# Optimization experiments

Hardware: AMD Instinct MI355X
Metric: run time of the kernel (lower is better)

Reference implementation:

```python
import jax, jax.numpy as jnp
import numpy as np

N_NODES = 100000
N_EDGES = 1600000
IN_F = 128
OUT_F = 128
HID = 2 * OUT_F  # 256


def setup_inputs() -> dict:
    key = jax.random.key(0)
    k1, k2, k3, k4, k5 = jax.random.split(key, 5)
    x = jax.random.normal(k1, (N_NODES, IN_F), dtype=jnp.float32)
    src = jax.random.randint(k2, (N_EDGES,), 0, N_NODES, dtype=jnp.int64)
    dst = jax.random.randint(k3, (N_EDGES,), 0, N_NODES, dtype=jnp.int64)
    # GraphConv params: glorot-style init, zero bias (as in dgl defaults)
    W1 = jax.random.normal(k4, (IN_F, HID), dtype=jnp.float32) / np.sqrt(IN_F)
    b1 = jnp.zeros((HID,), dtype=jnp.float32)
    W2 = jax.random.normal(k5, (HID, OUT_F), dtype=jnp.float32) / np.sqrt(HID)
    b2 = jnp.zeros((OUT_F,), dtype=jnp.float32)
    return {"x": x, "W1": W1, "b1": b1, "W2": W2, "b2": b2, "src": src, "dst": dst}


def _degree_norms(src, dst):
    ones = jnp.ones(src.shape[0], dtype=jnp.float32)
    out_deg = jax.ops.segment_sum(ones, src, num_segments=N_NODES)
    in_deg = jax.ops.segment_sum(ones, dst, num_segments=N_NODES)
    # dgl norm='both': deg^{-1/2}, with 0-degree clamped to 1
    out_norm = jnp.where(out_deg > 0, out_deg, 1.0) ** -0.5
    in_norm = jnp.where(in_deg > 0, in_deg, 1.0) ** -0.5
    return out_norm, in_norm


def _graph_conv(x, W, b, src, dst, out_norm, in_norm):
    # dgl GraphConv, norm='both': apply weight first if in_feats > out_feats
    h = x * out_norm[:, None]
    if W.shape[0] > W.shape[1]:
        h = h @ W                       # [N, out] -- shrink before aggregation
        agg = jax.ops.segment_sum(h[src], dst, num_segments=N_NODES)
        return agg * in_norm[:, None] + b
    else:
        agg = jax.ops.segment_sum(h[src], dst, num_segments=N_NODES)
        return (agg * in_norm[:, None]) @ W + b


def reference(x, W1, b1, W2, b2, src, dst):
    out_norm, in_norm = _degree_norms(src, dst)
    h = jax.nn.relu(_graph_conv(x, W1, b1, src, dst, out_norm, in_norm))
    h = jax.nn.relu(_graph_conv(h, W2, b2, src, dst, out_norm, in_norm))
    return h
```

## Files before the change

kernel.cpp:

```cpp
#include <hip/hip_runtime.h>
#include <stdint.h>

#define NNODES 100000
#define NEDGES 1600000
#define NBIN 391
#define EPB 4096
#define NB 391

typedef unsigned short bf16_t;
typedef __attribute__((ext_vector_type(8))) short bf16x8;
typedef __attribute__((ext_vector_type(8))) unsigned short u16x8;
typedef __attribute__((ext_vector_type(4))) float f32x4;

__device__ __forceinline__ float bf2f(unsigned short u) {
  return __uint_as_float(((unsigned)u) << 16);
}
__device__ __forceinline__ unsigned short f2bf(float f) {
  unsigned u = __float_as_uint(f);
  return (unsigned short)((u + 0x7FFFu + ((u >> 16) & 1u)) >> 16);
}
__device__ __forceinline__ void gload_lds16(const void* g, void* lds) {
  __builtin_amdgcn_global_load_lds(
      (const __attribute__((address_space(1))) unsigned int*)g,
      (__attribute__((address_space(3))) unsigned int*)lds, 16, 0, 0);
}

__global__ __launch_bounds__(256) void hist2_kernel(
    const int* __restrict__ src, const int* __restrict__ dst,
    int* __restrict__ cntD, int* __restrict__ cntS) {
  __shared__ int hD[NBIN], hS[NBIN];
  int blk = blockIdx.x, t = threadIdx.x;
  for (int i = t; i < NBIN; i += 256) { hD[i] = 0; hS[i] = 0; }
  __syncthreads();
  int e0 = blk * EPB + t * 16;
  if (e0 + 15 < NEDGES) {
#pragma unroll
    for (int q = 0; q < 4; q++) {
      int4 s4 = *reinterpret_cast<const int4*>(src + e0 + q * 4);
      int4 d4 = *reinterpret_cast<const int4*>(dst + e0 + q * 4);
      atomicAdd(&hD[d4.x >> 8], 1); atomicAdd(&hS[s4.x >> 8], 1);
      atomicAdd(&hD[d4.y >> 8], 1); atomicAdd(&hS[s4.y >> 8], 1);
      atomicAdd(&hD[d4.z >> 8], 1); atomicAdd(&hS[s4.z >> 8], 1);
      atomicAdd(&hD[d4.w >> 8], 1); atomicAdd(&hS[s4.w >> 8], 1);
    }
  } else {
    for (int e = e0; e < NEDGES && e < e0 + 16; e++) {
      atomicAdd(&hD[dst[e] >> 8], 1);
      atomicAdd(&hS[src[e] >> 8], 1);
    }
  }
  __syncthreads();
  for (int i = t; i < NBIN; i += 256) {
    cntD[(size_t)blk * NBIN + i] = hD[i];
    cntS[(size_t)blk * NBIN + i] = hS[i];
  }
}

__global__ __launch_bounds__(512) void scan_bin_kernel(
    int* __restrict__ cntD, int* __restrict__ cntS, int* __restrict__ binTot) {
  __shared__ int lds[512];
  int g = blockIdx.x, t = threadIdx.x;
  int* cnt = (g < NBIN) ? cntD : cntS;
  int gg = (g < NBIN) ? g : g - NBIN;
  int v = (t < NB) ? cnt[(size_t)t * NBIN + gg] : 0;
  lds[t] = v;
  __syncthreads();
  for (int off = 1; off < 512; off <<= 1) {
    int a = (t >= off) ? lds[t - off] : 0;
    __syncthreads();
    lds[t] += a;
    __syncthreads();
  }
  if (t < NB) cnt[(size_t)t * NBIN + gg] = lds[t] - v;
  if (t == 0) binTot[g] = lds[511];
}

__global__ __launch_bounds__(512) void base_wcast_kernel(
    const int* __restrict__ binTot, int* __restrict__ binbaseD,
    int* __restrict__ binbaseS, int* __restrict__ row_ptr,
    const float* __restrict__ W1, const float* __restrict__ W2,
    bf16_t* __restrict__ W1t, bf16_t* __restrict__ W2t) {
  if (blockIdx.x == 0) {
    __shared__ int lds[512];
    int t = threadIdx.x;
    int v = (t < NBIN) ? binTot[t] : 0;
    lds[t] = v;
    __syncthreads();
    for (int off = 1; off < 512; off <<= 1) {
      int a = (t >= off) ? lds[t - off] : 0;
      __syncthreads();
      lds[t] += a;
      __syncthreads();
    }
    if (t < NBIN) binbaseD[t] = lds[t] - v;
    if (t == NBIN - 1) { binbaseD[NBIN] = lds[t]; row_ptr[NNODES] = lds[t]; }
    __syncthreads();
    int v2 = (t < NBIN) ? binTot[NBIN + t] : 0;
    lds[t] = v2;
    __syncthreads();
    for (int off = 1; off < 512; off <<= 1) {
      int a = (t >= off) ? lds[t - off] : 0;
      __syncthreads();
      lds[t] += a;
      __syncthreads();
    }
    if (t < NBIN) binbaseS[t] = lds[t] - v2;
    if (t == NBIN - 1) binbaseS[NBIN] = lds[t];
  } else {
    int i = (blockIdx.x - 1) * 512 + threadIdx.x;
    if (i < 32768) {
      int n = i / 128, k = i % 128;
      W1t[i] = f2bf(W1[(size_t)k * 256 + n]);
    } else if (i < 65536) {
      int j = i - 32768;
      int n = j / 256, k = j % 256;
      W2t[j] = f2bf(W2[(size_t)k * 128 + n]);
    }
  }
}

__global__ __launch_bounds__(256) void scatter_recs_kernel(
    const int* __restrict__ src, const int* __restrict__ dst,
    const int* __restrict__ cntD, const int* __restrict__ cntS,
    const int* __restrict__ binbaseD, const int* __restrict__ binbaseS,
    unsigned int* __restrict__ recD, unsigned char* __restrict__ recS) {
  __shared__ int cD[NBIN], cS[NBIN];
  int blk = blockIdx.x, t = threadIdx.x;
  for (int i = t; i < NBIN; i += 256) {
    cD[i] = binbaseD[i] + cntD[(size_t)blk * NBIN + i];
    cS[i] = binbaseS[i] + cntS[(size_t)blk * NBIN + i];
  }
  __syncthreads();
  int e0 = blk * EPB + t * 16;
  if (e0 + 15 < NEDGES) {
#pragma unroll
    for (int q = 0; q < 4; q++) {
      int4 s4 = *reinterpret_cast<const int4*>(src + e0 + q * 4);
      int4 d4 = *reinterpret_cast<const int4*>(dst + e0 + q * 4);
      int ss[4] = {s4.x, s4.y, s4.z, s4.w};
      int dd[4] = {d4.x, d4.y, d4.z, d4.w};
#pragma unroll
      for (int i = 0; i < 4; i++) {
        int s = ss[i], d = dd[i];
        int pos = atomicAdd(&cD[d >> 8], 1);
        recD[pos] = ((unsigned)s << 8) | (unsigned)(d & 255);
        int ps = atomicAdd(&cS[s >> 8], 1);
        recS[ps] = (unsigned char)(s & 255);
      }
    }
  } else {
    for (int e = e0; e < NEDGES && e < e0 + 16; e++) {
      int s = src[e], d = dst[e];
      int pos = atomicAdd(&cD[d >> 8], 1);
      recD[pos] = ((unsigned)s << 8) | (unsigned)(d & 255);
      int ps = atomicAdd(&cS[s >> 8], 1);
      recS[ps] = (unsigned char)(s & 255);
    }
  }
}

__global__ __launch_bounds__(512) void finish2_kernel(
    const unsigned int* __restrict__ recD, const int* __restrict__ binbaseD,
    const unsigned char* __restrict__ recS, const int* __restrict__ binbaseS,
    int* __restrict__ row_ptr, float* __restrict__ in_norm, int* __restrict__ csr,
    float* __restrict__ out_norm, const float* __restrict__ x, bf16_t* __restrict__ xb) {
  __shared__ int hist[4096];
  __shared__ int cur[4096];
  __shared__ int sc[512];
  __shared__ float onv[256];
  int t = threadIdx.x;
  if (blockIdx.x < NBIN) {
    int b = blockIdx.x;
    int base = binbaseD[b];
    int cnt = binbaseD[b + 1] - base;
    for (int i = t; i < 4096; i += 512) hist[i] = 0;
    __syncthreads();
    const unsigned int* rec = recD + base;
    for (int i = t; i < cnt; i += 512) {
      unsigned int r = rec[i];
      atomicAdd(&hist[((r & 255u) << 4) | (r >> 21)], 1);
    }
    __syncthreads();
    int loc[8];
    int lsum = 0;
#pragma unroll
    for (int i = 0; i < 8; i++) { loc[i] = lsum; lsum += hist[t * 8 + i]; }
    sc[t] = lsum;
    __syncthreads();
    for (int off = 1; off < 512; off <<= 1) {
      int a = (t >= off) ? sc[t - off] : 0;
      __syncthreads();
      sc[t] += a;
      __syncthreads();
    }
    int toff = sc[t] - lsum;
#pragma unroll
    for (int i = 0; i < 8; i++) cur[t * 8 + i] = base + toff + loc[i];
    __syncthreads();
    if (t < 256) {
      int n = (b << 8) + t;
      if (n < NNODES) {
        row_ptr[n] = cur[t * 16];
        int v = 0;
#pragma unroll
        for (int p = 0; p < 16; p++) v += hist[t * 16 + p];
        in_norm[n] = rsqrtf((float)(v > 0 ? v : 1));
      }
    }
    __syncthreads();
    for (int i = t; i < cnt; i += 512) {
      unsigned int r = rec[i];
      int key = ((r & 255u) << 4) | (r >> 21);
      int slot = atomicAdd(&cur[key], 1);
      csr[slot] = (int)(r >> 8);
    }
  } else {
    int b = blockIdx.x - NBIN;
    int base = binbaseS[b];
    int cnt = binbaseS[b + 1] - base;
    if (t < 256) hist[t] = 0;
    __syncthreads();
    const unsigned char* rec = recS + base;
    for (int i = t; i < cnt; i += 512) atomicAdd(&hist[rec[i]], 1);
    __syncthreads();
    int n0 = b << 8;
    if (t < 256) {
      int v = hist[t];
      float on = rsqrtf((float)(v > 0 ? v : 1));
      onv[t] = on;
      int n = n0 + t;
      if (n < NNODES) out_norm[n] = on;
    }
    __syncthreads();
    for (int idx = t; idx < 256 * 16; idx += 512) {
      int r16 = idx >> 4, chunk = idx & 15;
      int n = n0 + r16;
      if (n >= NNODES) break;
      float s = onv[r16];
      const float4* xp = reinterpret_cast<const float4*>(x + (size_t)n * 128 + chunk * 8);
      float4 v0 = xp[0], v1 = xp[1];
      u16x8 u;
      u[0] = f2bf(v0.x * s); u[1] = f2bf(v0.y * s); u[2] = f2bf(v0.z * s); u[3] = f2bf(v0.w * s);
      u[4] = f2bf(v1.x * s); u[5] = f2bf(v1.y * s); u[6] = f2bf(v1.z * s); u[7] = f2bf(v1.w * s);
      *reinterpret_cast<u16x8*>(xb + (size_t)n * 128 + chunk * 8) = u;
    }
  }
}

template <int FIN>
__global__ __launch_bounds__(256) void gather_kernel(
    const bf16_t* __restrict__ feat, const int* __restrict__ row_ptr,
    const int* __restrict__ csr, const float* __restrict__ rs,
    const float* __restrict__ bias, void* __restrict__ outp) {
  int node = blockIdx.x * 16 + (threadIdx.x >> 4);
  int lane = threadIdx.x & 15;
  int start = row_ptr[node];
  int end = row_ptr[node + 1];
  float a[8];
#pragma unroll
  for (int t = 0; t < 8; t++) a[t] = 0.f;
  int j = start;
  for (; j + 7 < end; j += 8) {
    int4 sa = *reinterpret_cast<const int4*>(csr + j);
    int4 sb = *reinterpret_cast<const int4*>(csr + j + 4);
    u16x8 u0 = *reinterpret_cast<const u16x8*>(feat + (size_t)sa.x * 128 + lane * 8);
    u16x8 u1 = *reinterpret_cast<const u16x8*>(feat + (size_t)sa.y * 128 + lane * 8);
    u16x8 u2 = *reinterpret_cast<const u16x8*>(feat + (size_t)sa.z * 128 + lane * 8);
    u16x8 u3 = *reinterpret_cast<const u16x8*>(feat + (size_t)sa.w * 128 + lane * 8);
    u16x8 u4 = *reinterpret_cast<const u16x8*>(feat + (size_t)sb.x * 128 + lane * 8);
    u16x8 u5 = *reinterpret_cast<const u16x8*>(feat + (size_t)sb.y * 128 + lane * 8);
    u16x8 u6 = *reinterpret_cast<const u16x8*>(feat + (size_t)sb.z * 128 + lane * 8);
    u16x8 u7 = *reinterpret_cast<const u16x8*>(feat + (size_t)sb.w * 128 + lane * 8);
#pragma unroll
    for (int t = 0; t < 8; t++)
      a[t] += ((bf2f((unsigned short)u0[t]) + bf2f((unsigned short)u1[t])) +
               (bf2f((unsigned short)u2[t]) + bf2f((unsigned short)u3[t]))) +
              ((bf2f((unsigned short)u4[t]) + bf2f((unsigned short)u5[t])) +
               (bf2f((unsigned short)u6[t]) + bf2f((unsigned short)u7[t])));
  }
  if (j + 3 < end) {
    int4 sa = *reinterpret_cast<const int4*>(csr + j);
    u16x8 u0 = *reinterpret_cast<const u16x8*>(feat + (size_t)sa.x * 128 + lane * 8);
    u16x8 u1 = *reinterpret_cast<const u16x8*>(feat + (size_t)sa.y * 128 + lane * 8);
    u16x8 u2 = *reinterpret_cast<const u16x8*>(feat + (size_t)sa.z * 128 + lane * 8);
    u16x8 u3 = *reinterpret_cast<const u16x8*>(feat + (size_t)sa.w * 128 + lane * 8);
#pragma unroll
    for (int t = 0; t < 8; t++)
      a[t] += (bf2f((unsigned short)u0[t]) + bf2f((unsigned short)u1[t])) +
              (bf2f((unsigned short)u2[t]) + bf2f((unsigned short)u3[t]));
    j += 4;
  }
  for (; j < end; j++) {
    int s0 = csr[j];
    u16x8 u0 = *reinterpret_cast<const u16x8*>(feat + (size_t)s0 * 128 + lane * 8);
#pragma unroll
    for (int t = 0; t < 8; t++) a[t] += bf2f((unsigned short)u0[t]);
  }
  if (FIN == 0) {
    u16x8 o;
#pragma unroll
    for (int t = 0; t < 8; t++) o[t] = f2bf(a[t]);
    *reinterpret_cast<u16x8*>((bf16_t*)outp + (size_t)node * 128 + lane * 8) = o;
  } else {
    float s = rs[node];
    const float* bp = bias + lane * 8;
    float4 o0, o1;
    o0.x = fmaxf(fmaf(a[0], s, bp[0]), 0.f);
    o0.y = fmaxf(fmaf(a[1], s, bp[1]), 0.f);
    o0.z = fmaxf(fmaf(a[2], s, bp[2]), 0.f);
    o0.w = fmaxf(fmaf(a[3], s, bp[3]), 0.f);
    o1.x = fmaxf(fmaf(a[4], s, bp[4]), 0.f);
    o1.y = fmaxf(fmaf(a[5], s, bp[5]), 0.f);
    o1.z = fmaxf(fmaf(a[6], s, bp[6]), 0.f);
    o1.w = fmaxf(fmaf(a[7], s, bp[7]), 0.f);
    float* op = (float*)outp + (size_t)node * 128 + lane * 8;
    *reinterpret_cast<float4*>(op) = o0;
    *reinterpret_cast<float4*>(op + 4) = o1;
  }
}

__global__ __launch_bounds__(256) void gemm12_kernel(
    const bf16_t* __restrict__ A,
    const bf16_t* __restrict__ W1t,
    const bf16_t* __restrict__ W2t,
    const float* __restrict__ b1,
    const float* __restrict__ in_norm,
    const float* __restrict__ out_norm,
    bf16_t* __restrict__ s2b) {
  __shared__ __align__(16) bf16_t As[64 * 128];
  __shared__ __align__(16) bf16_t Wb[128 * 128];
  __shared__ __align__(16) bf16_t H[64 * 256];

  const int tid = threadIdx.x;
  const int lane = tid & 63;
  const int w = tid >> 6;
  const int m0 = blockIdx.x * 64;
  const int l15 = lane & 15;
  const int S = lane >> 4;
  const int r = w * 16 + l15;
  const int lr0 = w * 16 + S * 4;

#pragma unroll
  for (int p = 0; p < 4; p++) {
    int pos = p * 256 + tid;
    int rr = pos >> 4, slot = pos & 15;
    int row = m0 + rr; if (row > NNODES - 1) row = NNODES - 1;
    int ko = (slot ^ (rr & 7)) << 3;
    gload_lds16(A + (size_t)row * 128 + ko, &As[(p * 256 + w * 64) * 8]);
  }
#pragma unroll
  for (int p = 0; p < 8; p++) {
    int pos = p * 256 + tid;
    int n = pos >> 4, slot = pos & 15;
    int ko = (slot ^ (n & 7)) << 3;
    gload_lds16(W1t + (size_t)n * 128 + ko, &Wb[(p * 256 + w * 64) * 8]);
  }
  __syncthreads();

  float inn[4];
#pragma unroll
  for (int reg = 0; reg < 4; reg++) {
    int grow = m0 + lr0 + reg;
    inn[reg] = (grow < NNODES) ? in_norm[grow] : 1.0f;
  }

#pragma unroll
  for (int h = 0; h < 2; h++) {
    if (h == 1) {
      __syncthreads();
#pragma unroll
      for (int p = 0; p < 8; p++) {
        int pos = p * 256 + tid;
        int n = pos >> 4, slot = pos & 15;
        int ko = (slot ^ (n & 7)) << 3;
        gload_lds16(W1t + (size_t)(128 + n) * 128 + ko, &Wb[(p * 256 + w * 64) * 8]);
      }
      __syncthreads();
    }
    f32x4 acc1[8];
#pragma unroll
    for (int fn = 0; fn < 8; fn++) acc1[fn] = (f32x4){0.f, 0.f, 0.f, 0.f};
#pragma unroll
    for (int kk8 = 0; kk8 < 16; kk8 += 4) {
      bf16x8 af = *reinterpret_cast<const bf16x8*>(&As[r * 128 + (((kk8 + S) ^ (r & 7)) << 3)]);
#pragma unroll
      for (int fn = 0; fn < 8; fn++) {
        int n = fn * 16 + l15;
        bf16x8 bf = *reinterpret_cast<const bf16x8*>(&Wb[n * 128 + (((kk8 + S) ^ (n & 7)) << 3)]);
        acc1[fn] = __builtin_amdgcn_mfma_f32_16x16x32_bf16(af, bf, acc1[fn], 0, 0, 0);
      }
    }
#pragma unroll
    for (int fn = 0; fn < 8; fn++) {
      int col = h * 128 + fn * 16 + l15;
      float bb = b1[col];
#pragma unroll
      for (int reg = 0; reg < 4; reg++) {
        int lr = lr0 + reg;
        float v = fmaxf(fmaf(acc1[fn][reg], inn[reg], bb), 0.f);
        int slot = (col >> 3) ^ (lr & 7);
        H[lr * 256 + slot * 8 + (col & 7)] = f2bf(v);
      }
    }
  }
  __syncthreads();

  f32x4 acc2[8];
#pragma unroll
  for (int fn = 0; fn < 8; fn++) acc2[fn] = (f32x4){0.f, 0.f, 0.f, 0.f};
#pragma unroll
  for (int kh = 0; kh < 2; kh++) {
#pragma unroll
    for (int p = 0; p < 8; p++) {
      int pos = p * 256 + tid;
      int n = pos >> 4, slot = pos & 15;
      int ko = kh * 128 + ((slot ^ (n & 7)) << 3);
      gload_lds16(W2t + (size_t)n * 256 + ko, &Wb[(p * 256 + w * 64) * 8]);
    }
    __syncthreads();
#pragma unroll
    for (int kk8 = 0; kk8 < 16; kk8 += 4) {
      int oct = kh * 16 + kk8 + S;
      bf16x8 af = *reinterpret_cast<const bf16x8*>(&H[r * 256 + ((oct ^ (r & 7)) << 3)]);
#pragma unroll
      for (int fn = 0; fn < 8; fn++) {
        int n = fn * 16 + l15;
        bf16x8 bf = *reinterpret_cast<const bf16x8*>(&Wb[n * 128 + (((kk8 + S) ^ (n & 7)) << 3)]);
        acc2[fn] = __builtin_amdgcn_mfma_f32_16x16x32_bf16(af, bf, acc2[fn], 0, 0, 0);
      }
    }
    __syncthreads();
  }

  float onr[4];
#pragma unroll
  for (int reg = 0; reg < 4; reg++) {
    int grow = m0 + lr0 + reg;
    onr[reg] = (grow < NNODES) ? out_norm[grow] : 0.0f;
  }
#pragma unroll
  for (int fn = 0; fn < 8; fn++) {
    int col = fn * 16 + l15;
#pragma unroll
    for (int reg = 0; reg < 4; reg++) {
      int lr = lr0 + reg;
      As[lr * 128 + col] = f2bf(acc2[fn][reg] * onr[reg]);
    }
  }
  __syncthreads();
#pragma unroll
  for (int p = 0; p < 4; p++) {
    int pos = p * 256 + tid;
    int rr = pos >> 4;
    int cc = (pos & 15) * 8;
    int grow = m0 + rr;
    if (grow < NNODES)
      *reinterpret_cast<u16x8*>(s2b + (size_t)grow * 128 + cc) =
          *reinterpret_cast<const u16x8*>(&As[rr * 128 + cc]);
  }
}

extern "C" void kernel_launch(void* const* d_in, const int* in_sizes, int n_in,
                              void* d_out, int out_size, void* d_ws, size_t ws_size,
                              hipStream_t stream) {
  const float* x  = (const float*)d_in[0];
  const float* W1 = (const float*)d_in[1];
  const float* b1 = (const float*)d_in[2];
  const float* W2 = (const float*)d_in[3];
  const float* b2 = (const float*)d_in[4];
  const int* src  = (const int*)d_in[5];
  const int* dst  = (const int*)d_in[6];
  float* out = (float*)d_out;

  char* ws = (char*)d_ws;
  int*           cntD     = (int*)          (ws + 0);
  int*           cntS     = (int*)          (ws + 700000);
  int*           binTot   = (int*)          (ws + 1400000);
  int*           binbaseD = (int*)          (ws + 1404000);
  int*           binbaseS = (int*)          (ws + 1406000);
  int*           row_ptr  = (int*)          (ws + 1408000);
  float*         out_norm = (float*)        (ws + 1810000);
  float*         in_norm  = (float*)        (ws + 2210000);
  bf16_t*        W1t      = (bf16_t*)       (ws + 2610000);
  bf16_t*        W2t      = (bf16_t*)       (ws + 2675536);
  unsigned int*  recD     = (unsigned int*) (ws + 2741072);
  unsigned char* recS     = (unsigned char*)(ws + 9141072);
  int*           csr      = (int*)          (ws + 10741072);
  bf16_t*        xb       = (bf16_t*)       (ws + 17141072);
  bf16_t*        agg1     = (bf16_t*)       (ws + 42741072);
  bf16_t*        s2b      = xb;

  hist2_kernel<<<NB, 256, 0, stream>>>(src, dst, cntD, cntS);
  scan_bin_kernel<<<2 * NBIN, 512, 0, stream>>>(cntD, cntS, binTot);
  base_wcast_kernel<<<129, 512, 0, stream>>>(binTot, binbaseD, binbaseS, row_ptr, W1, W2, W1t, W2t);
  scatter_recs_kernel<<<NB, 256, 0, stream>>>(src, dst, cntD, cntS, binbaseD, binbaseS, recD, recS);
  finish2_kernel<<<2 * NBIN, 512, 0, stream>>>(recD, binbaseD, recS, binbaseS,
                                               row_ptr, in_norm, csr, out_norm, x, xb);

  gather_kernel<0><<<NNODES / 16, 256, 0, stream>>>(xb, row_ptr, csr, nullptr, nullptr, agg1);

  gemm12_kernel<<<(NNODES + 63) / 64, 256, 0, stream>>>(agg1, W1t, W2t, b1, in_norm, out_norm, s2b);

  gather_kernel<1><<<NNODES / 16, 256, 0, stream>>>(s2b, row_ptr, csr, in_norm, b2, out);
}
```

Before: 256.0 us.

## Stage block CSR indices in LDS and double-buffer neighbor gathers

The gather kernel now cooperatively loads each block's CSR neighbor indices into shared memory, falling back to global reads when a block has more than 2048 edges. The inner loop is software-pipelined with two register buffers of 8 neighbor rows, so loads for the next batch are issued before the current batch is summed. This aims to hide gather latency and cut redundant global index loads. It costs a __syncthreads, more registers (possibly lower occupancy), and 8 KB of LDS per block.

```diff
diff --git a/kernel.cpp b/kernel.cpp
--- a/kernel.cpp
+++ b/kernel.cpp
@@ -247,55 +247,136 @@
   }
 }
 
+template <typename F>
+__device__ __forceinline__ void gather_row(F idxf, const bf16_t* __restrict__ fb,
+                                           int start, int end, float* a) {
+  int j = start;
+  int nb = (end - start) >> 3;
+  if (nb > 0) {
+    int ia[8], ib[8];
+    u16x8 uA[8], uB[8];
+#pragma unroll
+    for (int t = 0; t < 8; t++) ia[t] = idxf(j + t);
+#pragma unroll
+    for (int t = 0; t < 8; t++)
+      uA[t] = *reinterpret_cast<const u16x8*>(fb + (size_t)ia[t] * 128);
+    j += 8;
+    int b = 1;
+    for (; b + 1 < nb; b += 2) {
+#pragma unroll
+      for (int t = 0; t < 8; t++) ib[t] = idxf(j + t);
+#pragma unroll
+      for (int t = 0; t < 8; t++)
+        uB[t] = *reinterpret_cast<const u16x8*>(fb + (size_t)ib[t] * 128);
+      j += 8;
+#pragma unroll
+      for (int f = 0; f < 8; f++) {
+        float s01 = bf2f((unsigned short)uA[0][f]) + bf2f((unsigned short)uA[1][f]);
+        float s23 = bf2f((unsigned short)uA[2][f]) + bf2f((unsigned short)uA[3][f]);
+        float s45 = bf2f((unsigned short)uA[4][f]) + bf2f((unsigned short)uA[5][f]);
+        float s67 = bf2f((unsigned short)uA[6][f]) + bf2f((unsigned short)uA[7][f]);
+        a[f] += (s01 + s23) + (s45 + s67);
+      }
+#pragma unroll
+      for (int t = 0; t < 8; t++) ia[t] = idxf(j + t);
+#pragma unroll
+      for (int t = 0; t < 8; t++)
+        uA[t] = *reinterpret_cast<const u16x8*>(fb + (size_t)ia[t] * 128);
+      j += 8;
+#pragma unroll
+      for (int f = 0; f < 8; f++) {
+        float s01 = bf2f((unsigned short)uB[0][f]) + bf2f((unsigned short)uB[1][f]);
+        float s23 = bf2f((unsigned short)uB[2][f]) + bf2f((unsigned short)uB[3][f]);
+        float s45 = bf2f((unsigned short)uB[4][f]) + bf2f((unsigned short)uB[5][f]);
+        float s67 = bf2f((unsigned short)uB[6][f]) + bf2f((unsigned short)uB[7][f]);
+        a[f] += (s01 + s23) + (s45 + s67);
+      }
+    }
+    if (b < nb) {
+#pragma unroll
+      for (int t = 0; t < 8; t++) ib[t] = idxf(j + t);
+#pragma unroll
+      for (int t = 0; t < 8; t++)
+        uB[t] = *reinterpret_cast<const u16x8*>(fb + (size_t)ib[t] * 128);
+      j += 8;
+#pragma unroll
+      for (int f = 0; f < 8; f++) {
+        float s01 = bf2f((unsigned short)uA[0][f]) + bf2f((unsigned short)uA[1][f]);
+        float s23 = bf2f((unsigned short)uA[2][f]) + bf2f((unsigned short)uA[3][f]);
+        float s45 = bf2f((unsigned short)uA[4][f]) + bf2f((unsigned short)uA[5][f]);
+        float s67 = bf2f((unsigned short)uA[6][f]) + bf2f((unsigned short)uA[7][f]);
+        a[f] += (s01 + s23) + (s45 + s67);
+      }
+#pragma unroll
+      for (int f = 0; f < 8; f++) {
+        float s01 = bf2f((unsigned short)uB[0][f]) + bf2f((unsigned short)uB[1][f]);
+        float s23 = bf2f((unsigned short)uB[2][f]) + bf2f((unsigned short)uB[3][f]);
+        float s45 = bf2f((unsigned short)uB[4][f]) + bf2f((unsigned short)uB[5][f]);
+        float s67 = bf2f((unsigned short)uB[6][f]) + bf2f((unsigned short)uB[7][f]);
+        a[f] += (s01 + s23) + (s45 + s67);
+      }
+    } else {
+#pragma unroll
+      for (int f = 0; f < 8; f++) {
+        float s01 = bf2f((unsigned short)uA[0][f]) + bf2f((unsigned short)uA[1][f]);
+        float s23 = bf2f((unsigned short)uA[2][f]) + bf2f((unsigned short)uA[3][f]);
+        float s45 = bf2f((unsigned short)uA[4][f]) + bf2f((unsigned short)uA[5][f]);
+        float s67 = bf2f((unsigned short)uA[6][f]) + bf2f((unsigned short)uA[7][f]);
+        a[f] += (s01 + s23) + (s45 + s67);
+      }
+    }
+  }
+  if (j + 3 < end) {
+    int i0 = idxf(j), i1 = idxf(j + 1), i2 = idxf(j + 2), i3 = idxf(j + 3);
+    u16x8 u0 = *reinterpret_cast<const u16x8*>(fb + (size_t)i0 * 128);
+    u16x8 u1 = *reinterpret_cast<const u16x8*>(fb + (size_t)i1 * 128);
+    u16x8 u2 = *reinterpret_cast<const u16x8*>(fb + (size_t)i2 * 128);
+    u16x8 u3 = *reinterpret_cast<const u16x8*>(fb + (size_t)i3 * 128);
+#pragma unroll
+    for (int f = 0; f < 8; f++)
+      a[f] += (bf2f((unsigned short)u0[f]) + bf2f((unsigned short)u1[f])) +
+              (bf2f((unsigned short)u2[f]) + bf2f((unsigned short)u3[f]));
+    j += 4;
+  }
+  for (; j < end; j++) {
+    int s0 = idxf(j);
+    u16x8 u0 = *reinterpret_cast<const u16x8*>(fb + (size_t)s0 * 128);
+#pragma unroll
+    for (int f = 0; f < 8; f++) a[f] += bf2f((unsigned short)u0[f]);
+  }
+}
+
 template <int FIN>
 __global__ __launch_bounds__(256) void gather_kernel(
     const bf16_t* __restrict__ feat, const int* __restrict__ row_ptr,
     const int* __restrict__ csr, const float* __restrict__ rs,
     const float* __restrict__ bias, void* __restrict__ outp) {
-  int node = blockIdx.x * 16 + (threadIdx.x >> 4);
+  __shared__ int sidx[2048];
+  int node0 = blockIdx.x * 16;
+  int node = node0 + (threadIdx.x >> 4);
   int lane = threadIdx.x & 15;
+  int blkStart = row_ptr[node0];
+  int blkEnd = row_ptr[node0 + 16];
+  int blkCnt = blkEnd - blkStart;
+  bool staged = (blkCnt <= 2048);
+  if (staged) {
+    for (int i = threadIdx.x; i < blkCnt; i += 256) sidx[i] = csr[blkStart + i];
+  }
+  __syncthreads();
+
   int start = row_ptr[node];
   int end = row_ptr[node + 1];
+  const bf16_t* fb = feat + (size_t)lane * 8;
   float a[8];
 #pragma unroll
   for (int t = 0; t < 8; t++) a[t] = 0.f;
-  int j = start;
-  for (; j + 7 < end; j += 8) {
-    int4 sa = *reinterpret_cast<const int4*>(csr + j);
-    int4 sb = *reinterpret_cast<const int4*>(csr + j + 4);
-    u16x8 u0 = *reinterpret_cast<const u16x8*>(feat + (size_t)sa.x * 128 + lane * 8);
-    u16x8 u1 = *reinterpret_cast<const u16x8*>(feat + (size_t)sa.y * 128 + lane * 8);
-    u16x8 u2 = *reinterpret_cast<const u16x8*>(feat + (size_t)sa.z * 128 + lane * 8);
-    u16x8 u3 = *reinterpret_cast<const u16x8*>(feat + (size_t)sa.w * 128 + lane * 8);
-    u16x8 u4 = *reinterpret_cast<const u16x8*>(feat + (size_t)sb.x * 128 + lane * 8);
-    u16x8 u5 = *reinterpret_cast<const u16x8*>(feat + (size_t)sb.y * 128 + lane * 8);
-    u16x8 u6 = *reinterpret_cast<const u16x8*>(feat + (size_t)sb.z * 128 + lane * 8);
-    u16x8 u7 = *reinterpret_cast<const u16x8*>(feat + (size_t)sb.w * 128 + lane * 8);
-#pragma unroll
-    for (int t = 0; t < 8; t++)
-      a[t] += ((bf2f((unsigned short)u0[t]) + bf2f((unsigned short)u1[t])) +
-               (bf2f((unsigned short)u2[t]) + bf2f((unsigned short)u3[t]))) +
-              ((bf2f((unsigned short)u4[t]) + bf2f((unsigned short)u5[t])) +
-               (bf2f((unsigned short)u6[t]) + bf2f((unsigned short)u7[t])));
-  }
-  if (j + 3 < end) {
-    int4 sa = *reinterpret_cast<const int4*>(csr + j);
-    u16x8 u0 = *reinterpret_cast<const u16x8*>(feat + (size_t)sa.x * 128 + lane * 8);
-    u16x8 u1 = *reinterpret_cast<const u16x8*>(feat + (size_t)sa.y * 128 + lane * 8);
-    u16x8 u2 = *reinterpret_cast<const u16x8*>(feat + (size_t)sa.z * 128 + lane * 8);
-    u16x8 u3 = *reinterpret_cast<const u16x8*>(feat + (size_t)sa.w * 128 + lane * 8);
-#pragma unroll
-    for (int t = 0; t < 8; t++)
-      a[t] += (bf2f((unsigned short)u0[t]) + bf2f((unsigned short)u1[t])) +
-              (bf2f((unsigned short)u2[t]) + bf2f((unsigned short)u3[t]));
-    j += 4;
-  }
-  for (; j < end; j++) {
-    int s0 = csr[j];
-    u16x8 u0 = *reinterpret_cast<const u16x8*>(feat + (size_t)s0 * 128 + lane * 8);
-#pragma unroll
-    for (int t = 0; t < 8; t++) a[t] += bf2f((unsigned short)u0[t]);
-  }
+
+  if (staged) {
+    gather_row([&](int j) { return sidx[j - blkStart]; }, fb, start, end, a);
+  } else {
+    gather_row([&](int j) { return csr[j]; }, fb, start, end, a);
+  }
+
   if (FIN == 0) {
     u16x8 o;
 #pragma unroll
```

Measured after the change: 259.8 us. No clear change (+1.5%).
